# Optimization experiments

Measured on AMD Instinct MI355X. Metric: run time of the kernel, lower is better.

Reference implementation:

```python
import jax, jax.numpy as jnp
import numpy as np

D_MODEL = 1024
N_HEADS = 16
D_HEAD = D_MODEL // N_HEADS
SCALE = 1.0 / np.sqrt(D_HEAD).astype(np.float32)


def _feature_map(x):
    # phi(x) = elu(x) + 1
    return jax.nn.elu(x) + 1.0


def setup_inputs() -> dict:
    key = jax.random.key(0)
    ks = jax.random.split(key, 7)
    b, s = 4, 2048
    w = 1.0 / np.sqrt(D_MODEL).astype(np.float32)
    return {
        "x": jax.random.normal(ks[0], (b, s, D_MODEL), dtype=jnp.float32),
        "Wq": jax.random.normal(ks[1], (D_MODEL, D_MODEL), dtype=jnp.float32) * w,
        "Wk": jax.random.normal(ks[2], (D_MODEL, D_MODEL), dtype=jnp.float32) * w,
        "Wv": jax.random.normal(ks[3], (D_MODEL, D_MODEL), dtype=jnp.float32) * w,
        "Wo": jax.random.normal(ks[4], (D_MODEL, D_MODEL), dtype=jnp.float32) * w,
        "Wg": jax.random.normal(ks[5], (N_HEADS, D_MODEL), dtype=jnp.float32) * w,
        "bg": jax.random.normal(ks[6], (N_HEADS,), dtype=jnp.float32) * 0.02,
    }


def reference(x, Wq, Wk, Wv, Wo, Wg, bg):
    b, s, _ = x.shape
    # projections (PyTorch Linear: y = x @ W.T)
    q = (x @ Wq.T).reshape(b, s, N_HEADS, D_HEAD)
    k = (x @ Wk.T).reshape(b, s, N_HEADS, D_HEAD)
    v = (x @ Wv.T).reshape(b, s, N_HEADS, D_HEAD)
    q = _feature_map(q * SCALE)
    k = _feature_map(k)
    gate = jax.nn.sigmoid(x @ Wg.T + bg)  # [b, s, h]

    # time-major for scan: [s, b, h, dh] and [s, b, h]
    qt = jnp.moveaxis(q, 1, 0)
    kt = jnp.moveaxis(k, 1, 0)
    vt = jnp.moveaxis(v, 1, 0)
    gt = jnp.moveaxis(gate, 1, 0)

    S0 = jnp.zeros((b, N_HEADS, D_HEAD, D_HEAD), dtype=x.dtype)

    def step(S, inp):
        q_t, k_t, v_t, g_t = inp
        # S_t = g_t * S_{t-1} + k_t v_t^T
        S = g_t[:, :, None, None] * S + k_t[..., :, None] * v_t[..., None, :]
        y_t = jnp.einsum("bhi,bhij->bhj", q_t, S)
        return S, y_t

    _, ys = jax.lax.scan(step, S0, (qt, kt, vt, gt))  # ys: [s, b, h, dh]
    y = jnp.moveaxis(ys, 0, 1).reshape(b, s, D_MODEL)
    return y @ Wo.T
```

## Files before the change

### kernel.cpp

```cpp
#include <hip/hip_runtime.h>
#include <hip/hip_bf16.h>
#include <math.h>

#define BATCH 4
#define SEQ 2048
#define DMODEL 1024
#define NHEADS 16
#define DHEAD 64
#define MTOK (BATCH * SEQ)
#define SCALE_Q 0.125f
#define NCHAIN (BATCH * NHEADS)
#define CT 64
#define NC (SEQ / CT)
#define SP 72
#define QKVS 3072

typedef unsigned short ushort_t;
typedef __attribute__((ext_vector_type(8))) short bf16x8;
typedef __attribute__((ext_vector_type(4))) float f32x4;

__device__ __forceinline__ float bf2f(unsigned short u) {
    return __uint_as_float(((unsigned)u) << 16);
}
__device__ __forceinline__ unsigned short f2bf(float f) {
    unsigned u = __float_as_uint(f);
    return (unsigned short)((u + 0x7fffu + ((u >> 16) & 1u)) >> 16);
}

__global__ __launch_bounds__(256) void cvt_f32_bf16(const float* __restrict__ in,
                                                    ushort_t* __restrict__ out, int n4) {
    int i = blockIdx.x * 256 + threadIdx.x;
    if (i < n4) {
        float4 v = ((const float4*)in)[i];
        ushort4 o;
        o.x = f2bf(v.x); o.y = f2bf(v.y); o.z = f2bf(v.z); o.w = f2bf(v.w);
        ((ushort4*)out)[i] = o;
    }
}

__global__ __launch_bounds__(256) void cvt_weights(const float* __restrict__ Wq,
                                                   const float* __restrict__ Wk,
                                                   const float* __restrict__ Wv,
                                                   const float* __restrict__ Wo,
                                                   ushort_t* __restrict__ dst) {
    int i = blockIdx.x * 256 + threadIdx.x;
    const int row = i >> 8;
    const int c4 = i & 255;
    const float* src;
    if (row < 1024)      src = Wq + (size_t)row * DMODEL;
    else if (row < 2048) src = Wk + (size_t)(row - 1024) * DMODEL;
    else if (row < 3072) src = Wv + (size_t)(row - 2048) * DMODEL;
    else                 src = Wo + (size_t)(row - 3072) * DMODEL;
    float4 v = ((const float4*)src)[c4];
    ushort4 o;
    o.x = f2bf(v.x); o.y = f2bf(v.y); o.z = f2bf(v.z); o.w = f2bf(v.w);
    ((ushort4*)(dst + (size_t)row * DMODEL))[c4] = o;
}

#define GT 128
#define GBK 32

__global__ __launch_bounds__(256) void gemm_bf16(const ushort_t* __restrict__ A,
                                                 const ushort_t* __restrict__ B,
                                                 float* __restrict__ Cf,
                                                 ushort_t* __restrict__ Cb,
                                                 int M, int N, int K,
                                                 int mode) {
    __shared__ ushort_t As[2][GT * GBK];
    __shared__ ushort_t Bs[2][GT * GBK];

    const int tid = threadIdx.x;
    const int w = tid >> 6;
    const int l = tid & 63;
    const int m0 = blockIdx.y * GT;
    const int n0 = blockIdx.x * GT;
    const int wm = (w >> 1) * 64;
    const int wn = (w & 1) * 64;

    const int srow = l >> 2;
    const int schunk = ((l & 3) ^ ((l >> 3) & 3)) * 8;

    const ushort_t* aseg[2];
    const ushort_t* bseg[2];
#pragma unroll
    for (int i = 0; i < 2; ++i) {
        const int s = w * 2 + i;
        aseg[i] = A + (size_t)(m0 + s * 16 + srow) * K + schunk;
        bseg[i] = B + (size_t)(n0 + s * 16 + srow) * K + schunk;
    }

#define STAGE(buf, k0)                                                          \
    do {                                                                        \
        _Pragma("unroll")                                                       \
        for (int i_ = 0; i_ < 2; ++i_) {                                        \
            const int s_ = w * 2 + i_;                                          \
            __builtin_amdgcn_global_load_lds(                                   \
                (const __attribute__((address_space(1))) unsigned int*)(const void*)(aseg[i_] + (k0)), \
                (__attribute__((address_space(3))) unsigned int*)(void*)&As[buf][s_ * 16 * GBK], \
                16, 0, 0);                                                      \
            __builtin_amdgcn_global_load_lds(                                   \
                (const __attribute__((address_space(1))) unsigned int*)(const void*)(bseg[i_] + (k0)), \
                (__attribute__((address_space(3))) unsigned int*)(void*)&Bs[buf][s_ * 16 * GBK], \
                16, 0, 0);                                                      \
        }                                                                       \
    } while (0)

    f32x4 acc[4][4];
#pragma unroll
    for (int i = 0; i < 4; ++i)
#pragma unroll
        for (int j = 0; j < 4; ++j)
#pragma unroll
            for (int r = 0; r < 4; ++r) acc[i][j][r] = 0.f;

    const int fr = l & 15;
    const int fsw = (((l >> 4) ^ ((fr >> 1) & 3))) * 8;

    STAGE(0, 0);

    const int nit = K / GBK;
    for (int it = 0; it < nit; ++it) {
        __syncthreads();
        if (it + 1 < nit) STAGE((it + 1) & 1, (it + 1) * GBK);

        const ushort_t* __restrict__ as = As[it & 1];
        const ushort_t* __restrict__ bs = Bs[it & 1];

        bf16x8 af[4], bfr[4];
#pragma unroll
        for (int ti = 0; ti < 4; ++ti)
            af[ti] = *(const bf16x8*)&as[(wm + ti * 16 + fr) * GBK + fsw];
#pragma unroll
        for (int tj = 0; tj < 4; ++tj)
            bfr[tj] = *(const bf16x8*)&bs[(wn + tj * 16 + fr) * GBK + fsw];
#pragma unroll
        for (int ti = 0; ti < 4; ++ti)
#pragma unroll
            for (int tj = 0; tj < 4; ++tj)
                acc[ti][tj] = __builtin_amdgcn_mfma_f32_16x16x32_bf16(
                    af[ti], bfr[tj], acc[ti][tj], 0, 0, 0);
    }
#undef STAGE

    float escale = 1.0f;
    bool do_phi = false;
    if (mode == 3) {
        do_phi = (n0 < 2048);
        escale = (n0 < 1024) ? SCALE_Q : 1.0f;
    }

    const int er = (l >> 4) * 4;
    const int ec = l & 15;
#pragma unroll
    for (int ti = 0; ti < 4; ++ti)
#pragma unroll
        for (int tj = 0; tj < 4; ++tj)
#pragma unroll
            for (int r = 0; r < 4; ++r) {
                const int row = m0 + wm + ti * 16 + er + r;
                const int col = n0 + wn + tj * 16 + ec;
                float val = acc[ti][tj][r];
                if (mode == 0) {
                    Cf[(size_t)row * N + col] = val;
                } else {
                    val *= escale;
                    if (do_phi) val = (val > 0.f) ? (val + 1.f) : __expf(val);
                    Cb[(size_t)row * N + col] = f2bf(val);
                }
            }
}

__global__ __launch_bounds__(256) void gate_kernel(const float* __restrict__ x,
                                                   const float* __restrict__ Wg,
                                                   const float* __restrict__ bg,
                                                   float* __restrict__ gate) {
    const int m = blockIdx.x;
    const int tid = threadIdx.x;
    const int h = tid >> 4;
    const int r = tid & 15;

    const float* xr = x + (size_t)m * DMODEL;
    const float* wr = Wg + (size_t)h * DMODEL;

    float p = 0.f;
#pragma unroll
    for (int i = 0; i < 16; ++i) {
        const int k = (r << 2) + (i << 6);
        float4 xv = *(const float4*)&xr[k];
        float4 wv = *(const float4*)&wr[k];
        p += xv.x * wv.x + xv.y * wv.y + xv.z * wv.z + xv.w * wv.w;
    }
    p += __shfl_xor(p, 8, 64);
    p += __shfl_xor(p, 4, 64);
    p += __shfl_xor(p, 2, 64);
    p += __shfl_xor(p, 1, 64);
    if (r == 0) {
        float vv = p + bg[h];
        gate[(size_t)m * NHEADS + h] = 1.f / (1.f + __expf(-vv));
    }
}

__global__ __launch_bounds__(256) void p1_kernel(const ushort_t* __restrict__ qkv,
                                                 const float* __restrict__ gate,
                                                 float* __restrict__ Dt,
                                                 float* __restrict__ Bg) {
    const int tile = blockIdx.x;
    const int chain = tile >> 5;
    const int c = tile & 31;
    const int b = chain >> 4;
    const int h = chain & 15;
    const int tid = threadIdx.x;
    const int w = tid >> 6;
    const int l = tid & 63;

    __shared__ ushort_t Ks[CT * SP];
    __shared__ ushort_t Vs[CT * SP];
    __shared__ float bs[CT];

    {
        const int row = tid >> 2;
        const int seg = (tid & 3) * 16;
        const size_t grow = ((size_t)(b * SEQ + c * CT + row)) * QKVS + h * DHEAD + seg;
        float4 a0 = *(const float4*)&qkv[grow + 1024];
        float4 a1 = *(const float4*)&qkv[grow + 1024 + 8];
        float4 b0 = *(const float4*)&qkv[grow + 2048];
        float4 b1 = *(const float4*)&qkv[grow + 2048 + 8];
        *(float4*)&Ks[row * SP + seg]     = a0;
        *(float4*)&Ks[row * SP + seg + 8] = a1;
        *(float4*)&Vs[row * SP + seg]     = b0;
        *(float4*)&Vs[row * SP + seg + 8] = b1;
    }
    if (tid < 64) {
        float g = gate[((size_t)(b * SEQ + c * CT + tid)) * NHEADS + h];
        float lg = __logf(g);
#pragma unroll
        for (int d = 1; d < 64; d <<= 1) {
            float n = __shfl_up(lg, d, 64);
            if (l >= d) lg += n;
        }
        bs[tid] = lg;
        if (tid == 63) Bg[tile] = lg;
    }
    __syncthreads();

    const float B = bs[63];
    const int fr = l & 15;
    const int fq = (l >> 4) * 8;
    const int jw = w * 16;

    f32x4 accD[4];
#pragma unroll
    for (int nt = 0; nt < 4; ++nt)
#pragma unroll
        for (int r = 0; r < 4; ++r) accD[nt][r] = 0.f;

#pragma unroll
    for (int kc = 0; kc < 2; ++kc) {
        float ef[8];
#pragma unroll
        for (int m = 0; m < 8; ++m) ef[m] = __expf(B - bs[kc * 32 + fq + m]);
        bf16x8 va;
#pragma unroll
        for (int m = 0; m < 8; ++m)
            va[m] = (short)Vs[(kc * 32 + fq + m) * SP + jw + fr];
#pragma unroll
        for (int nt = 0; nt < 4; ++nt) {
            bf16x8 kf;
#pragma unroll
            for (int m = 0; m < 8; ++m)
                kf[m] = (short)f2bf(ef[m] * bf2f(Ks[(kc * 32 + fq + m) * SP + nt * 16 + fr]));
            accD[nt] = __builtin_amdgcn_mfma_f32_16x16x32_bf16(va, kf, accD[nt], 0, 0, 0);
        }
    }

    const int er = (l >> 4) * 4;
    const size_t dbase = (size_t)tile * (DHEAD * DHEAD);
#pragma unroll
    for (int nt = 0; nt < 4; ++nt)
#pragma unroll
        for (int r = 0; r < 4; ++r) {
            const int j = jw + er + r;
            const int i = nt * 16 + fr;
            Dt[dbase + j * DHEAD + i] = accD[nt][r];
        }
}

__global__ __launch_bounds__(256) void p2_kernel(const float* __restrict__ Dt,
                                                 const float* __restrict__ Bg,
                                                 ushort_t* __restrict__ St) {
    const int chain = blockIdx.x >> 2;
    const int jq = (blockIdx.x & 3) * 16;
    const int tid = threadIdx.x;
    const int jj = jq + (tid >> 4);
    const int ii = (tid & 15) * 4;

    float4 S = make_float4(0.f, 0.f, 0.f, 0.f);
    for (int c = 0; c < NC; ++c) {
        const size_t base = (((size_t)chain * NC + c) * DHEAD + jj) * DHEAD + ii;
        ushort4 o;
        o.x = f2bf(S.x); o.y = f2bf(S.y); o.z = f2bf(S.z); o.w = f2bf(S.w);
        *(ushort4*)&St[base] = o;
        const float eB = __expf(Bg[chain * NC + c]);
        const float4 D = *(const float4*)&Dt[base];
        S.x = eB * S.x + D.x;
        S.y = eB * S.y + D.y;
        S.z = eB * S.z + D.z;
        S.w = eB * S.w + D.w;
    }
}

__global__ __launch_bounds__(256) void p3_kernel(const ushort_t* __restrict__ qkv,
                                                 const ushort_t* __restrict__ St,
                                                 const float* __restrict__ gate,
                                                 ushort_t* __restrict__ yb) {
    const int tile = blockIdx.x;
    const int chain = tile >> 5;
    const int c = tile & 31;
    const int b = chain >> 4;
    const int h = chain & 15;
    const int tid = threadIdx.x;
    const int w = tid >> 6;
    const int l = tid & 63;

    __shared__ ushort_t Qs[CT * SP];
    __shared__ ushort_t Ks[CT * SP];
    __shared__ ushort_t Vs[CT * SP];
    __shared__ ushort_t Ss[CT * SP];
    __shared__ ushort_t Ps[CT * SP];
    __shared__ float bs[CT];

    {
        const int row = tid >> 2;
        const int seg = (tid & 3) * 16;
        const size_t grow = ((size_t)(b * SEQ + c * CT + row)) * QKVS + h * DHEAD + seg;
        float4 q0 = *(const float4*)&qkv[grow];
        float4 q1 = *(const float4*)&qkv[grow + 8];
        float4 k0 = *(const float4*)&qkv[grow + 1024];
        float4 k1 = *(const float4*)&qkv[grow + 1024 + 8];
        float4 v0 = *(const float4*)&qkv[grow + 2048];
        float4 v1 = *(const float4*)&qkv[grow + 2048 + 8];
        const size_t srow = (((size_t)chain * NC + c) * DHEAD + row) * DHEAD + seg;
        float4 s0 = *(const float4*)&St[srow];
        float4 s1 = *(const float4*)&St[srow + 8];
        *(float4*)&Qs[row * SP + seg]     = q0;
        *(float4*)&Qs[row * SP + seg + 8] = q1;
        *(float4*)&Ks[row * SP + seg]     = k0;
        *(float4*)&Ks[row * SP + seg + 8] = k1;
        *(float4*)&Vs[row * SP + seg]     = v0;
        *(float4*)&Vs[row * SP + seg + 8] = v1;
        *(float4*)&Ss[row * SP + seg]     = s0;
        *(float4*)&Ss[row * SP + seg + 8] = s1;
    }
    if (tid < 64) {
        float g = gate[((size_t)(b * SEQ + c * CT + tid)) * NHEADS + h];
        float lg = __logf(g);
#pragma unroll
        for (int d = 1; d < 64; d <<= 1) {
            float n = __shfl_up(lg, d, 64);
            if (l >= d) lg += n;
        }
        bs[tid] = lg;
    }
    __syncthreads();

    const int fr = l & 15;
    const int fq = (l >> 4) * 8;
    const int tw = w * 16;

    bf16x8 qa[2];
#pragma unroll
    for (int kc = 0; kc < 2; ++kc)
        qa[kc] = *(const bf16x8*)&Qs[(tw + fr) * SP + kc * 32 + fq];

    f32x4 accA[4], accP[4];
#pragma unroll
    for (int nt = 0; nt < 4; ++nt)
#pragma unroll
        for (int r = 0; r < 4; ++r) { accA[nt][r] = 0.f; accP[nt][r] = 0.f; }

#pragma unroll
    for (int kc = 0; kc < 2; ++kc)
#pragma unroll
        for (int nt = 0; nt < 4; ++nt) {
            bf16x8 sb = *(const bf16x8*)&Ss[(nt * 16 + fr) * SP + kc * 32 + fq];
            accA[nt] = __builtin_amdgcn_mfma_f32_16x16x32_bf16(qa[kc], sb, accA[nt], 0, 0, 0);
            bf16x8 kf = *(const bf16x8*)&Ks[(nt * 16 + fr) * SP + kc * 32 + fq];
            accP[nt] = __builtin_amdgcn_mfma_f32_16x16x32_bf16(qa[kc], kf, accP[nt], 0, 0, 0);
        }

    const int er = (l >> 4) * 4;
    int trow[4];
    float bt[4];
#pragma unroll
    for (int r = 0; r < 4; ++r) { trow[r] = tw + er + r; bt[r] = bs[trow[r]]; }
#pragma unroll
    for (int nt = 0; nt < 4; ++nt) {
        const int tau = nt * 16 + fr;
        const float btau = bs[tau];
#pragma unroll
        for (int r = 0; r < 4; ++r) {
            float f = (tau <= trow[r]) ? __expf(bt[r] - btau) : 0.f;
            Ps[trow[r] * SP + tau] = f2bf(accP[nt][r] * f);
        }
    }
    __syncthreads();

    f32x4 accY[4];
#pragma unroll
    for (int r = 0; r < 4; ++r) {
        const float eb = __expf(bt[r]);
#pragma unroll
        for (int nt = 0; nt < 4; ++nt) accY[nt][r] = accA[nt][r] * eb;
    }
#pragma unroll
    for (int kc = 0; kc < 2; ++kc) {
        bf16x8 pa = *(const bf16x8*)&Ps[(tw + fr) * SP + kc * 32 + fq];
#pragma unroll
        for (int nt = 0; nt < 4; ++nt) {
            bf16x8 vf;
#pragma unroll
            for (int m = 0; m < 8; ++m)
                vf[m] = (short)Vs[(kc * 32 + fq + m) * SP + nt * 16 + fr];
            accY[nt] = __builtin_amdgcn_mfma_f32_16x16x32_bf16(pa, vf, accY[nt], 0, 0, 0);
        }
    }

    const size_t ybase = ((size_t)(b * SEQ + c * CT)) * DMODEL + h * DHEAD;
#pragma unroll
    for (int nt = 0; nt < 4; ++nt)
#pragma unroll
        for (int r = 0; r < 4; ++r)
            yb[ybase + (size_t)trow[r] * DMODEL + nt * 16 + fr] = f2bf(accY[nt][r]);
}

extern "C" void kernel_launch(void* const* d_in, const int* in_sizes, int n_in,
                              void* d_out, int out_size, void* d_ws, size_t ws_size,
                              hipStream_t stream) {
    const float* x  = (const float*)d_in[0];
    const float* Wq = (const float*)d_in[1];
    const float* Wk = (const float*)d_in[2];
    const float* Wv = (const float*)d_in[3];
    const float* Wo = (const float*)d_in[4];
    const float* Wg = (const float*)d_in[5];
    const float* bg = (const float*)d_in[6];
    float* out = (float*)d_out;

    const size_t elems = (size_t)MTOK * DMODEL;
    const size_t welems = (size_t)DMODEL * DMODEL;
    const size_t stelems = (size_t)NCHAIN * NC * DHEAD * DHEAD;

    ushort_t* xb   = (ushort_t*)d_ws;
    ushort_t* St   = xb;
    ushort_t* qkv  = xb + elems;
    ushort_t* wcat = qkv + (size_t)MTOK * QKVS;
    float* gate    = (float*)(wcat + 4 * welems);
    float* Bg      = gate + (size_t)MTOK * NHEADS;
    float* Dt      = Bg + (size_t)NCHAIN * NC;
    ushort_t* yb   = (ushort_t*)Dt;

    const size_t need = (size_t)((char*)(Dt + stelems) - (char*)d_ws);
    if (ws_size < need) return;

    cvt_f32_bf16<<<dim3((int)(elems / 4 / 256)), dim3(256), 0, stream>>>(x, xb, (int)(elems / 4));
    cvt_weights<<<dim3((int)(4 * welems / 4 / 256)), dim3(256), 0, stream>>>(Wq, Wk, Wv, Wo, wcat);

    gemm_bf16<<<dim3(QKVS / GT, MTOK / GT), dim3(256), 0, stream>>>(
        xb, wcat, nullptr, qkv, MTOK, QKVS, DMODEL, 3);

    gate_kernel<<<dim3(MTOK), dim3(256), 0, stream>>>(x, Wg, bg, gate);

    p1_kernel<<<dim3(NCHAIN * NC), dim3(256), 0, stream>>>(qkv, gate, Dt, Bg);
    p2_kernel<<<dim3(NCHAIN * 4), dim3(256), 0, stream>>>(Dt, Bg, St);
    p3_kernel<<<dim3(NCHAIN * NC), dim3(256), 0, stream>>>(qkv, St, gate, yb);

    gemm_bf16<<<dim3(DMODEL / GT, MTOK / GT), dim3(256), 0, stream>>>(
        yb, wcat + 3 * welems, out, nullptr, MTOK, DMODEL, DMODEL, 0);
}
```

Measured before the change: 268.2 us.

## Use 32x32 MFMA in GEMM, fuse x conversion with gate, drop a p3 barrier

The GEMM inner loop switches from 16x16x32 bf16 MFMAs on a 4x4 fragment grid to 32x32x16 MFMAs on a 2x2 grid, with matching swizzled LDS reads and a new epilogue mapping. The aim is fewer fragment loads and instructions per k-step. The x-to-bf16 conversion and the gate projection are fused into one per-token kernel so x is read once and one launch is saved. A __syncthreads between writing and reading the P tile in the chunk kernel is removed. This relies on each wave reading only the rows it wrote itself, which risks ordering problems in LDS.

New measurement: 272.7 us. No clear change (+1.7%).

```diff
diff --git a/kernel.cpp b/kernel.cpp
--- a/kernel.cpp
+++ b/kernel.cpp
@@ -18,6 +18,7 @@
 typedef unsigned short ushort_t;
 typedef __attribute__((ext_vector_type(8))) short bf16x8;
 typedef __attribute__((ext_vector_type(4))) float f32x4;
+typedef __attribute__((ext_vector_type(16))) float f32x16;
 
 __device__ __forceinline__ float bf2f(unsigned short u) {
     return __uint_as_float(((unsigned)u) << 16);
@@ -27,14 +28,40 @@
     return (unsigned short)((u + 0x7fffu + ((u >> 16) & 1u)) >> 16);
 }
 
-__global__ __launch_bounds__(256) void cvt_f32_bf16(const float* __restrict__ in,
-                                                    ushort_t* __restrict__ out, int n4) {
-    int i = blockIdx.x * 256 + threadIdx.x;
-    if (i < n4) {
-        float4 v = ((const float4*)in)[i];
+__global__ __launch_bounds__(256) void cvt_x_gate(const float* __restrict__ x,
+                                                  const float* __restrict__ Wg,
+                                                  const float* __restrict__ bg,
+                                                  ushort_t* __restrict__ xb,
+                                                  float* __restrict__ gate) {
+    const int m = blockIdx.x;
+    const int tid = threadIdx.x;
+    const float* xr = x + (size_t)m * DMODEL;
+
+    {
+        float4 v = ((const float4*)xr)[tid];
         ushort4 o;
         o.x = f2bf(v.x); o.y = f2bf(v.y); o.z = f2bf(v.z); o.w = f2bf(v.w);
-        ((ushort4*)out)[i] = o;
+        ((ushort4*)(xb + (size_t)m * DMODEL))[tid] = o;
+    }
+
+    const int h = tid >> 4;
+    const int r = tid & 15;
+    const float* wr = Wg + (size_t)h * DMODEL;
+    float p = 0.f;
+#pragma unroll
+    for (int i = 0; i < 16; ++i) {
+        const int k = (r << 2) + (i << 6);
+        float4 xv = *(const float4*)&xr[k];
+        float4 wv = *(const float4*)&wr[k];
+        p += xv.x * wv.x + xv.y * wv.y + xv.z * wv.z + xv.w * wv.w;
+    }
+    p += __shfl_xor(p, 8, 64);
+    p += __shfl_xor(p, 4, 64);
+    p += __shfl_xor(p, 2, 64);
+    p += __shfl_xor(p, 1, 64);
+    if (r == 0) {
+        float vv = p + bg[h];
+        gate[(size_t)m * NHEADS + h] = 1.f / (1.f + __expf(-vv));
     }
 }
 
@@ -105,16 +132,17 @@
         }                                                                       \
     } while (0)
 
-    f32x4 acc[4][4];
-#pragma unroll
-    for (int i = 0; i < 4; ++i)
-#pragma unroll
-        for (int j = 0; j < 4; ++j)
-#pragma unroll
-            for (int r = 0; r < 4; ++r) acc[i][j][r] = 0.f;
-
-    const int fr = l & 15;
-    const int fsw = (((l >> 4) ^ ((fr >> 1) & 3))) * 8;
+    f32x16 acc[2][2];
+#pragma unroll
+    for (int i = 0; i < 2; ++i)
+#pragma unroll
+        for (int j = 0; j < 2; ++j)
+#pragma unroll
+            for (int r = 0; r < 16; ++r) acc[i][j][r] = 0.f;
+
+    const int fr32 = l & 31;
+    const int khalf = l >> 5;
+    const int swm = (fr32 >> 1) & 3;
 
     STAGE(0, 0);
 
@@ -126,19 +154,23 @@
         const ushort_t* __restrict__ as = As[it & 1];
         const ushort_t* __restrict__ bs = Bs[it & 1];
 
-        bf16x8 af[4], bfr[4];
-#pragma unroll
-        for (int ti = 0; ti < 4; ++ti)
-            af[ti] = *(const bf16x8*)&as[(wm + ti * 16 + fr) * GBK + fsw];
-#pragma unroll
-        for (int tj = 0; tj < 4; ++tj)
-            bfr[tj] = *(const bf16x8*)&bs[(wn + tj * 16 + fr) * GBK + fsw];
-#pragma unroll
-        for (int ti = 0; ti < 4; ++ti)
-#pragma unroll
-            for (int tj = 0; tj < 4; ++tj)
-                acc[ti][tj] = __builtin_amdgcn_mfma_f32_16x16x32_bf16(
-                    af[ti], bfr[tj], acc[ti][tj], 0, 0, 0);
+        bf16x8 af[2][2], bfr[2][2];
+#pragma unroll
+        for (int ti = 0; ti < 2; ++ti)
+#pragma unroll
+            for (int h = 0; h < 2; ++h) {
+                const int ss = (h * 2 + khalf) ^ swm;
+                af[ti][h] = *(const bf16x8*)&as[(wm + ti * 32 + fr32) * GBK + ss * 8];
+                bfr[ti][h] = *(const bf16x8*)&bs[(wn + ti * 32 + fr32) * GBK + ss * 8];
+            }
+#pragma unroll
+        for (int ti = 0; ti < 2; ++ti)
+#pragma unroll
+            for (int tj = 0; tj < 2; ++tj)
+#pragma unroll
+                for (int h = 0; h < 2; ++h)
+                    acc[ti][tj] = __builtin_amdgcn_mfma_f32_32x32x16_bf16(
+                        af[ti][h], bfr[tj][h], acc[ti][tj], 0, 0, 0);
     }
 #undef STAGE
 
@@ -149,16 +181,14 @@
         escale = (n0 < 1024) ? SCALE_Q : 1.0f;
     }
 
-    const int er = (l >> 4) * 4;
-    const int ec = l & 15;
-#pragma unroll
-    for (int ti = 0; ti < 4; ++ti)
-#pragma unroll
-        for (int tj = 0; tj < 4; ++tj)
-#pragma unroll
-            for (int r = 0; r < 4; ++r) {
-                const int row = m0 + wm + ti * 16 + er + r;
-                const int col = n0 + wn + tj * 16 + ec;
+#pragma unroll
+    for (int ti = 0; ti < 2; ++ti)
+#pragma unroll
+        for (int tj = 0; tj < 2; ++tj)
+#pragma unroll
+            for (int r = 0; r < 16; ++r) {
+                const int row = m0 + wm + ti * 32 + (r & 3) + 8 * (r >> 2) + 4 * khalf;
+                const int col = n0 + wn + tj * 32 + fr32;
                 float val = acc[ti][tj][r];
                 if (mode == 0) {
                     Cf[(size_t)row * N + col] = val;
@@ -168,36 +198,6 @@
                     Cb[(size_t)row * N + col] = f2bf(val);
                 }
             }
-}
-
-__global__ __launch_bounds__(256) void gate_kernel(const float* __restrict__ x,
-                                                   const float* __restrict__ Wg,
-                                                   const float* __restrict__ bg,
-                                                   float* __restrict__ gate) {
-    const int m = blockIdx.x;
-    const int tid = threadIdx.x;
-    const int h = tid >> 4;
-    const int r = tid & 15;
-
-    const float* xr = x + (size_t)m * DMODEL;
-    const float* wr = Wg + (size_t)h * DMODEL;
-
-    float p = 0.f;
-#pragma unroll
-    for (int i = 0; i < 16; ++i) {
-        const int k = (r << 2) + (i << 6);
-        float4 xv = *(const float4*)&xr[k];
-        float4 wv = *(const float4*)&wr[k];
-        p += xv.x * wv.x + xv.y * wv.y + xv.z * wv.z + xv.w * wv.w;
-    }
-    p += __shfl_xor(p, 8, 64);
-    p += __shfl_xor(p, 4, 64);
-    p += __shfl_xor(p, 2, 64);
-    p += __shfl_xor(p, 1, 64);
-    if (r == 0) {
-        float vv = p + bg[h];
-        gate[(size_t)m * NHEADS + h] = 1.f / (1.f + __expf(-vv));
-    }
 }
 
 __global__ __launch_bounds__(256) void p1_kernel(const ushort_t* __restrict__ qkv,
@@ -403,7 +403,6 @@
             Ps[trow[r] * SP + tau] = f2bf(accP[nt][r] * f);
         }
     }
-    __syncthreads();
 
     f32x4 accY[4];
 #pragma unroll
@@ -461,13 +460,11 @@
     const size_t need = (size_t)((char*)(Dt + stelems) - (char*)d_ws);
     if (ws_size < need) return;
 
-    cvt_f32_bf16<<<dim3((int)(elems / 4 / 256)), dim3(256), 0, stream>>>(x, xb, (int)(elems / 4));
+    cvt_x_gate<<<dim3(MTOK), dim3(256), 0, stream>>>(x, Wg, bg, xb, gate);
     cvt_weights<<<dim3((int)(4 * welems / 4 / 256)), dim3(256), 0, stream>>>(Wq, Wk, Wv, Wo, wcat);
 
     gemm_bf16<<<dim3(QKVS / GT, MTOK / GT), dim3(256), 0, stream>>>(
         xb, wcat, nullptr, qkv, MTOK, QKVS, DMODEL, 3);
-
-    gate_kernel<<<dim3(MTOK), dim3(256), 0, stream>>>(x, Wg, bg, gate);
 
     p1_kernel<<<dim3(NCHAIN * NC), dim3(256), 0, stream>>>(qkv, gate, Dt, Bg);
     p2_kernel<<<dim3(NCHAIN * 4), dim3(256), 0, stream>>>(Dt, Bg, St);
```

## Fuse prep kernels and stage K/V transposed in shared memory for vector fragment loads

Applied to the files above, without the earlier changes.

Merges the x cast, weight cast and gate projection into one kernel so x is read once and two launches are saved. In p1 and p3, K and V are written transposed into shared memory (with K pre-scaled by the decay factor in p1), so MFMA operand fragments become single 128-bit LDS loads instead of eight strided scalar reads plus repeated exp and conversion. A barrier before the P·V stage in p3 is removed, relying on each wave reading only its own rows of Ps. The transposed stores are scalar strided LDS writes that may add bank conflicts.

After: 267.2 us. No clear change (-0.4%).

```diff
diff --git a/kernel.cpp b/kernel.cpp
--- a/kernel.cpp
+++ b/kernel.cpp
@@ -27,34 +27,59 @@
     return (unsigned short)((u + 0x7fffu + ((u >> 16) & 1u)) >> 16);
 }
 
-__global__ __launch_bounds__(256) void cvt_f32_bf16(const float* __restrict__ in,
-                                                    ushort_t* __restrict__ out, int n4) {
-    int i = blockIdx.x * 256 + threadIdx.x;
-    if (i < n4) {
-        float4 v = ((const float4*)in)[i];
+__global__ __launch_bounds__(256) void cvt_all(const float* __restrict__ x,
+                                               const float* __restrict__ Wq,
+                                               const float* __restrict__ Wk,
+                                               const float* __restrict__ Wv,
+                                               const float* __restrict__ Wo,
+                                               const float* __restrict__ Wg,
+                                               const float* __restrict__ bg,
+                                               ushort_t* __restrict__ xb,
+                                               ushort_t* __restrict__ wcat,
+                                               float* __restrict__ gate) {
+    const int blk = blockIdx.x;
+    const int tid = threadIdx.x;
+
+    if (blk < MTOK) {
+        const int m = blk;
+        const float* xr = x + (size_t)m * DMODEL;
+        {
+            float4 v = ((const float4*)xr)[tid];
+            ushort4 o;
+            o.x = f2bf(v.x); o.y = f2bf(v.y); o.z = f2bf(v.z); o.w = f2bf(v.w);
+            ((ushort4*)(xb + (size_t)m * DMODEL))[tid] = o;
+        }
+        const int h = tid >> 4;
+        const int r = tid & 15;
+        const float* wr = Wg + (size_t)h * DMODEL;
+        float p = 0.f;
+#pragma unroll
+        for (int i = 0; i < 16; ++i) {
+            const int k = (r << 2) + (i << 6);
+            float4 xv = *(const float4*)&xr[k];
+            float4 wv = *(const float4*)&wr[k];
+            p += xv.x * wv.x + xv.y * wv.y + xv.z * wv.z + xv.w * wv.w;
+        }
+        p += __shfl_xor(p, 8, 64);
+        p += __shfl_xor(p, 4, 64);
+        p += __shfl_xor(p, 2, 64);
+        p += __shfl_xor(p, 1, 64);
+        if (r == 0) {
+            float vv = p + bg[h];
+            gate[(size_t)m * NHEADS + h] = 1.f / (1.f + __expf(-vv));
+        }
+    } else {
+        const int row = blk - MTOK;
+        const float* src;
+        if (row < 1024)      src = Wq + (size_t)row * DMODEL;
+        else if (row < 2048) src = Wk + (size_t)(row - 1024) * DMODEL;
+        else if (row < 3072) src = Wv + (size_t)(row - 2048) * DMODEL;
+        else                 src = Wo + (size_t)(row - 3072) * DMODEL;
+        float4 v = ((const float4*)src)[tid];
         ushort4 o;
         o.x = f2bf(v.x); o.y = f2bf(v.y); o.z = f2bf(v.z); o.w = f2bf(v.w);
-        ((ushort4*)out)[i] = o;
-    }
-}
-
-__global__ __launch_bounds__(256) void cvt_weights(const float* __restrict__ Wq,
-                                                   const float* __restrict__ Wk,
-                                                   const float* __restrict__ Wv,
-                                                   const float* __restrict__ Wo,
-                                                   ushort_t* __restrict__ dst) {
-    int i = blockIdx.x * 256 + threadIdx.x;
-    const int row = i >> 8;
-    const int c4 = i & 255;
-    const float* src;
-    if (row < 1024)      src = Wq + (size_t)row * DMODEL;
-    else if (row < 2048) src = Wk + (size_t)(row - 1024) * DMODEL;
-    else if (row < 3072) src = Wv + (size_t)(row - 2048) * DMODEL;
-    else                 src = Wo + (size_t)(row - 3072) * DMODEL;
-    float4 v = ((const float4*)src)[c4];
-    ushort4 o;
-    o.x = f2bf(v.x); o.y = f2bf(v.y); o.z = f2bf(v.z); o.w = f2bf(v.w);
-    ((ushort4*)(dst + (size_t)row * DMODEL))[c4] = o;
+        ((ushort4*)(wcat + (size_t)row * DMODEL))[tid] = o;
+    }
 }
 
 #define GT 128
@@ -170,36 +195,6 @@
             }
 }
 
-__global__ __launch_bounds__(256) void gate_kernel(const float* __restrict__ x,
-                                                   const float* __restrict__ Wg,
-                                                   const float* __restrict__ bg,
-                                                   float* __restrict__ gate) {
-    const int m = blockIdx.x;
-    const int tid = threadIdx.x;
-    const int h = tid >> 4;
-    const int r = tid & 15;
-
-    const float* xr = x + (size_t)m * DMODEL;
-    const float* wr = Wg + (size_t)h * DMODEL;
-
-    float p = 0.f;
-#pragma unroll
-    for (int i = 0; i < 16; ++i) {
-        const int k = (r << 2) + (i << 6);
-        float4 xv = *(const float4*)&xr[k];
-        float4 wv = *(const float4*)&wr[k];
-        p += xv.x * wv.x + xv.y * wv.y + xv.z * wv.z + xv.w * wv.w;
-    }
-    p += __shfl_xor(p, 8, 64);
-    p += __shfl_xor(p, 4, 64);
-    p += __shfl_xor(p, 2, 64);
-    p += __shfl_xor(p, 1, 64);
-    if (r == 0) {
-        float vv = p + bg[h];
-        gate[(size_t)m * NHEADS + h] = 1.f / (1.f + __expf(-vv));
-    }
-}
-
 __global__ __launch_bounds__(256) void p1_kernel(const ushort_t* __restrict__ qkv,
                                                  const float* __restrict__ gate,
                                                  float* __restrict__ Dt,
@@ -213,23 +208,19 @@
     const int w = tid >> 6;
     const int l = tid & 63;
 
-    __shared__ ushort_t Ks[CT * SP];
-    __shared__ ushort_t Vs[CT * SP];
+    __shared__ ushort_t Kt[DHEAD * SP];
+    __shared__ ushort_t Vt[DHEAD * SP];
     __shared__ float bs[CT];
 
-    {
-        const int row = tid >> 2;
-        const int seg = (tid & 3) * 16;
-        const size_t grow = ((size_t)(b * SEQ + c * CT + row)) * QKVS + h * DHEAD + seg;
-        float4 a0 = *(const float4*)&qkv[grow + 1024];
-        float4 a1 = *(const float4*)&qkv[grow + 1024 + 8];
-        float4 b0 = *(const float4*)&qkv[grow + 2048];
-        float4 b1 = *(const float4*)&qkv[grow + 2048 + 8];
-        *(float4*)&Ks[row * SP + seg]     = a0;
-        *(float4*)&Ks[row * SP + seg + 8] = a1;
-        *(float4*)&Vs[row * SP + seg]     = b0;
-        *(float4*)&Vs[row * SP + seg + 8] = b1;
-    }
+    const int tau = tid >> 2;
+    const int seg = (tid & 3) * 16;
+    const size_t grow = ((size_t)(b * SEQ + c * CT + tau)) * QKVS + h * DHEAD + seg;
+    union { float4 f4[2]; ushort_t us[16]; } uk, uv;
+    uk.f4[0] = *(const float4*)&qkv[grow + 1024];
+    uk.f4[1] = *(const float4*)&qkv[grow + 1024 + 8];
+    uv.f4[0] = *(const float4*)&qkv[grow + 2048];
+    uv.f4[1] = *(const float4*)&qkv[grow + 2048 + 8];
+
     if (tid < 64) {
         float g = gate[((size_t)(b * SEQ + c * CT + tid)) * NHEADS + h];
         float lg = __logf(g);
@@ -243,7 +234,14 @@
     }
     __syncthreads();
 
-    const float B = bs[63];
+    const float e = __expf(bs[63] - bs[tau]);
+#pragma unroll
+    for (int f = 0; f < 16; ++f) {
+        Kt[(seg + f) * SP + tau] = f2bf(e * bf2f(uk.us[f]));
+        Vt[(seg + f) * SP + tau] = uv.us[f];
+    }
+    __syncthreads();
+
     const int fr = l & 15;
     const int fq = (l >> 4) * 8;
     const int jw = w * 16;
@@ -256,19 +254,10 @@
 
 #pragma unroll
     for (int kc = 0; kc < 2; ++kc) {
-        float ef[8];
-#pragma unroll
-        for (int m = 0; m < 8; ++m) ef[m] = __expf(B - bs[kc * 32 + fq + m]);
-        bf16x8 va;
-#pragma unroll
-        for (int m = 0; m < 8; ++m)
-            va[m] = (short)Vs[(kc * 32 + fq + m) * SP + jw + fr];
+        bf16x8 va = *(const bf16x8*)&Vt[(jw + fr) * SP + kc * 32 + fq];
 #pragma unroll
         for (int nt = 0; nt < 4; ++nt) {
-            bf16x8 kf;
-#pragma unroll
-            for (int m = 0; m < 8; ++m)
-                kf[m] = (short)f2bf(ef[m] * bf2f(Ks[(kc * 32 + fq + m) * SP + nt * 16 + fr]));
+            bf16x8 kf = *(const bf16x8*)&Kt[(nt * 16 + fr) * SP + kc * 32 + fq];
             accD[nt] = __builtin_amdgcn_mfma_f32_16x16x32_bf16(va, kf, accD[nt], 0, 0, 0);
         }
     }
@@ -324,7 +313,7 @@
 
     __shared__ ushort_t Qs[CT * SP];
     __shared__ ushort_t Ks[CT * SP];
-    __shared__ ushort_t Vs[CT * SP];
+    __shared__ ushort_t Vt[DHEAD * SP];
     __shared__ ushort_t Ss[CT * SP];
     __shared__ ushort_t Ps[CT * SP];
     __shared__ float bs[CT];
@@ -337,8 +326,9 @@
         float4 q1 = *(const float4*)&qkv[grow + 8];
         float4 k0 = *(const float4*)&qkv[grow + 1024];
         float4 k1 = *(const float4*)&qkv[grow + 1024 + 8];
-        float4 v0 = *(const float4*)&qkv[grow + 2048];
-        float4 v1 = *(const float4*)&qkv[grow + 2048 + 8];
+        union { float4 f4[2]; ushort_t us[16]; } uv;
+        uv.f4[0] = *(const float4*)&qkv[grow + 2048];
+        uv.f4[1] = *(const float4*)&qkv[grow + 2048 + 8];
         const size_t srow = (((size_t)chain * NC + c) * DHEAD + row) * DHEAD + seg;
         float4 s0 = *(const float4*)&St[srow];
         float4 s1 = *(const float4*)&St[srow + 8];
@@ -346,10 +336,11 @@
         *(float4*)&Qs[row * SP + seg + 8] = q1;
         *(float4*)&Ks[row * SP + seg]     = k0;
         *(float4*)&Ks[row * SP + seg + 8] = k1;
-        *(float4*)&Vs[row * SP + seg]     = v0;
-        *(float4*)&Vs[row * SP + seg + 8] = v1;
         *(float4*)&Ss[row * SP + seg]     = s0;
         *(float4*)&Ss[row * SP + seg + 8] = s1;
+#pragma unroll
+        for (int f = 0; f < 16; ++f)
+            Vt[(seg + f) * SP + row] = uv.us[f];
     }
     if (tid < 64) {
         float g = gate[((size_t)(b * SEQ + c * CT + tid)) * NHEADS + h];
@@ -403,7 +394,6 @@
             Ps[trow[r] * SP + tau] = f2bf(accP[nt][r] * f);
         }
     }
-    __syncthreads();
 
     f32x4 accY[4];
 #pragma unroll
@@ -417,10 +407,7 @@
         bf16x8 pa = *(const bf16x8*)&Ps[(tw + fr) * SP + kc * 32 + fq];
 #pragma unroll
         for (int nt = 0; nt < 4; ++nt) {
-            bf16x8 vf;
-#pragma unroll
-            for (int m = 0; m < 8; ++m)
-                vf[m] = (short)Vs[(kc * 32 + fq + m) * SP + nt * 16 + fr];
+            bf16x8 vf = *(const bf16x8*)&Vt[(nt * 16 + fr) * SP + kc * 32 + fq];
             accY[nt] = __builtin_amdgcn_mfma_f32_16x16x32_bf16(pa, vf, accY[nt], 0, 0, 0);
         }
     }
@@ -461,13 +448,11 @@
     const size_t need = (size_t)((char*)(Dt + stelems) - (char*)d_ws);
     if (ws_size < need) return;
 
-    cvt_f32_bf16<<<dim3((int)(elems / 4 / 256)), dim3(256), 0, stream>>>(x, xb, (int)(elems / 4));
-    cvt_weights<<<dim3((int)(4 * welems / 4 / 256)), dim3(256), 0, stream>>>(Wq, Wk, Wv, Wo, wcat);
+    cvt_all<<<dim3(MTOK + 4096), dim3(256), 0, stream>>>(x, Wq, Wk, Wv, Wo, Wg, bg,
+                                                         xb, wcat, gate);
 
     gemm_bf16<<<dim3(QKVS / GT, MTOK / GT), dim3(256), 0, stream>>>(
         xb, wcat, nullptr, qkv, MTOK, QKVS, DMODEL, 3);
-
-    gate_kernel<<<dim3(MTOK), dim3(256), 0, stream>>>(x, Wg, bg, gate);
 
     p1_kernel<<<dim3(NCHAIN * NC), dim3(256), 0, stream>>>(qkv, gate, Dt, Bg);
     p2_kernel<<<dim3(NCHAIN * 4), dim3(256), 0, stream>>>(Dt, Bg, St);
```
